# Kernel optimization log

Measured on AMD Instinct MI355X. Metric: run time of the kernel, lower is better.

The kernel has to match this reference:

```python
import jax, jax.numpy as jnp
import numpy as np

B, C, H, G = 4, 128, 8, 64
F = G * G  # 4096 faces on a GxG grid mesh surrogate
DH = C // H


def _build_rings():
    # BFS rings on a GxG 4-neighbor grid from face 0 (corner): ring r = {(i,j): i+j == r}
    rings_list = []
    for r in range(2 * G - 1):
        lo, hi = max(0, r - G + 1), min(r, G - 1)
        rings_list.append([i * G + (r - i) for i in range(lo, hi + 1)])
    n_rings = len(rings_list)
    max_ring = max(len(rr) for rr in rings_list)
    rings = np.full((n_rings, max_ring), -1, dtype=np.int64)
    sizes = np.zeros((n_rings,), dtype=np.int64)
    for r, rr in enumerate(rings_list):
        rings[r, :len(rr)] = rr
        sizes[r] = len(rr)
    return rings, sizes


def setup_inputs() -> dict:
    key = jax.random.key(0)
    ks = jax.random.split(key, 6)
    s = 1.0 / np.sqrt(C)
    x = jax.random.normal(ks[0], (B, C, F), dtype=jnp.float32)
    Wq0 = jax.random.normal(ks[1], (C, C), dtype=jnp.float32) * s
    Wk0 = jax.random.normal(ks[2], (C, C), dtype=jnp.float32) * s
    Wv0 = jax.random.normal(ks[3], (C, C), dtype=jnp.float32) * s
    Wq1 = jax.random.normal(ks[4], (C, C), dtype=jnp.float32) * s
    Wk1 = jax.random.normal(ks[5], (C, C), dtype=jnp.float32) * s
    rings, sizes = _build_rings()
    return {"x": x, "Wq0": Wq0, "Wk0": Wk0, "Wv0": Wv0, "Wq1": Wq1, "Wk1": Wk1,
            "rings": jnp.asarray(rings), "ring_sizes": jnp.asarray(sizes)}


def _attend(q_in, kv_in, Wq, Wk, Wv):
    # AnchorAttentionBlock, mode='resid': MHA(q=q_in, kv=kv_in) + q_in
    Bq, Cc, Nq = q_in.shape
    Nk = kv_in.shape[2]
    q = jnp.einsum('oc,bcn->bon', Wq, q_in).reshape(Bq, H, DH, Nq)
    k = jnp.einsum('oc,bcn->bon', Wk, kv_in).reshape(Bq, H, DH, Nk)
    v = jnp.einsum('oc,bcn->bon', Wv, kv_in).reshape(Bq, H, DH, Nk)
    a = jax.nn.softmax(jnp.einsum('bhdq,bhdk->bhqk', q, k) / np.float32(np.sqrt(DH)), axis=-1)
    o = jnp.einsum('bhqk,bhdk->bhdq', a, v).reshape(Bq, Cc, Nq)
    return o + q_in


def _cos_map(q_in, kv_in, Wq, Wk):
    # return_map=True, normalize=True -> per-head cosine similarity map in [-1, 1]
    Bq, _, Nq = q_in.shape
    Nk = kv_in.shape[2]
    q = jnp.einsum('oc,bcn->bon', Wq, q_in).reshape(Bq, H, DH, Nq)
    k = jnp.einsum('oc,bcn->bon', Wk, kv_in).reshape(Bq, H, DH, Nk)
    qn = q * jax.lax.rsqrt(jnp.sum(q * q, axis=2, keepdims=True) + 1e-8)
    kn = k * jax.lax.rsqrt(jnp.sum(k * k, axis=2, keepdims=True) + 1e-8)
    return jnp.einsum('bhdq,bhdk->bhqk', qn, kn)  # [B,H,Nq,Nk]


def reference(x, Wq0, Wk0, Wv0, Wq1, Wk1, rings, ring_sizes):
    rings_np = np.asarray(rings)
    sizes_np = np.asarray(ring_sizes)
    feats = x
    # Sequential BFS flood-fill: per ring, boundary faces attend over all faces.
    # Vectorized over the batch (all meshes share the grid topology + anchor).
    for r in range(rings_np.shape[0]):
        ring = rings_np[r, :int(sizes_np[r])]          # concrete face indices of this ring
        bf = feats[:, :, ring]                          # [B, C, Nb] boundary features
        bf = _attend(bf, feats, Wq0, Wk0, Wv0)          # kv = all faces (current state)
        feats = feats.at[:, :, ring].set(bf)
    anchor = int(rings_np[0, 0])
    anchor_x = feats[:, :, anchor:anchor + 1]           # [B, C, 1]
    q_x = _attend(x, anchor_x, Wq0, Wk0, Wv0)           # attention[:-1] pass on raw x
    m = _cos_map(q_x, anchor_x, Wq1, Wk1)               # [B, H, F, 1] in [-1, 1]
    final_scores = jnp.mean((m + 1.0) * 0.5, axis=1)    # [B, F, 1] in [0, 1]
    return feats, final_scores
```

## Files before the change

### kernel.cpp

```cpp
#include <hip/hip_runtime.h>
#include <hip/hip_bf16.h>

#define Bn 4
#define Cn 128
#define Fn 4096
#define NRINGS 127

typedef short bhalf4 __attribute__((ext_vector_type(4)));
typedef float f32x4  __attribute__((ext_vector_type(4)));

#define OFF_K   1048576
#define OFF_V   2097152
#define OFF_PM  3145728
#define OFF_PL  3211264
#define OFF_PO  3276800
#define OFF_VA  4325376
#define OFF_KN  4325888

__device__ __forceinline__ ushort f2bf(float f) {
    __hip_bfloat16 h = __float2bfloat16(f);
    return *reinterpret_cast<ushort*>(&h);
}

__global__ __launch_bounds__(512, 2) void initQKV(
    const float* __restrict__ x, const float* __restrict__ Wq0,
    const float* __restrict__ Wk0, const float* __restrict__ Wv0,
    ushort* __restrict__ Q0bf, ushort* __restrict__ Kbf, ushort* __restrict__ Vbf)
{
    __shared__ float xs[Cn * 64];
    const int wg = blockIdx.x, t = threadIdx.x;
    const int b = wg >> 6, n0 = (wg & 63) << 6;
    for (int idx = t; idx < Cn * 64; idx += 512) {
        int c = idx >> 6, j = idx & 63;
        xs[idx] = x[(((b << 7) + c) << 12) + n0 + j];
    }
    __syncthreads();
    const int o = t & 127, j0 = (t >> 7) << 4;
    float aq[16], ak[16], av[16];
#pragma unroll
    for (int k = 0; k < 16; ++k) { aq[k] = 0.f; ak[k] = 0.f; av[k] = 0.f; }
    for (int c = 0; c < Cn; ++c) {
        float wq = Wq0[(o << 7) + c];
        float wk = Wk0[(o << 7) + c];
        float wv = Wv0[(o << 7) + c];
        const float* xr = &xs[(c << 6) + j0];
#pragma unroll
        for (int k = 0; k < 16; ++k) {
            float xv = xr[k];
            aq[k] += wq * xv; ak[k] += wk * xv; av[k] += wv * xv;
        }
    }
    const int h = o >> 4, d = o & 15;
    const int bh = (b << 3) + h;
#pragma unroll
    for (int k = 0; k < 16; ++k) {
        int col = n0 + j0 + k;
        int qi = ((bh << 12) + col) * 16 + d;
        Q0bf[qi] = f2bf(aq[k]);
        Kbf[qi]  = f2bf(ak[k]);
    }
    uint vv[8];
#pragma unroll
    for (int k2 = 0; k2 < 8; ++k2)
        vv[k2] = (uint)f2bf(av[2*k2]) | ((uint)f2bf(av[2*k2+1]) << 16);
    uint4* dst = (uint4*)&Vbf[(((bh << 4) + d) << 12) + n0 + j0];
    dst[0] = make_uint4(vv[0], vv[1], vv[2], vv[3]);
    dst[1] = make_uint4(vv[4], vv[5], vv[6], vv[7]);
}

template<bool TAIL>
__global__ __launch_bounds__(512, 2) void fusedRing(
    const float* __restrict__ x, const float* __restrict__ Wk0,
    const float* __restrict__ Wv0, const int* __restrict__ rings,
    const int* __restrict__ rsz, const ushort* __restrict__ Q0bf,
    ushort* __restrict__ Kbf, ushort* __restrict__ Vbf,
    float* __restrict__ pm, float* __restrict__ pl, float* __restrict__ po,
    float* __restrict__ feats, int r)
{
    __shared__ ushort Kls[512 * 24];
    __shared__ ushort Vls[16 * 520];
    __shared__ ushort Qls[64 * 24];
    __shared__ float  outc[4 * 128];
    __shared__ int colsC[64], colsF[64];
    __shared__ int ownIdx[64];
    __shared__ int ownCnt;

    const int t = threadIdx.x, wgid = blockIdx.x;
    const int b = wgid >> 6, h = (wgid >> 3) & 7, sp = wgid & 7;
    const int bh = (b << 3) + h;
    const int n  = TAIL ? 0 : rsz[r];
    const int np = (r > 0) ? rsz[r - 1] : 0;
    const int keybase = sp << 9;

    if (t < 64) colsC[t] = (r > 0 && t < np) ? rings[(r-1)*64 + t] : -1;
    else if (t < 128) { int q = t - 64; colsF[q] = (!TAIL && q < n) ? rings[r*64 + q] : -1; }
    if (t == 0) ownCnt = 0;
    __syncthreads();

    if (!TAIL) {
        {
            const uint4* src = (const uint4*)(Kbf + ((bh << 12) + keybase + t) * 16);
            uint4 a0 = src[0], a1 = src[1];
            *(uint4*)&Kls[t*24]     = a0;
            *(uint4*)&Kls[t*24 + 8] = a1;
        }
        {
            int d = t >> 5, c32 = t & 31;
            const uint4* src = (const uint4*)(Vbf + (((bh << 4) + d) << 12) + keybase + (c32 << 4));
            uint4 a0 = src[0], a1 = src[1];
            *(uint4*)&Vls[d*520 + (c32 << 4)]     = a0;
            *(uint4*)&Vls[d*520 + (c32 << 4) + 8] = a1;
        }
        if (t < 128) {
            int q = t >> 1, half = t & 1;
            int cq = colsF[q];
            uint4 qv = make_uint4(0u, 0u, 0u, 0u);
            if (cq >= 0)
                qv = *(const uint4*)(Q0bf + ((bh << 12) + cq) * 16 + half * 8);
            *(uint4*)&Qls[q*24 + half*8] = qv;
        }
    }
    __syncthreads();

    if (r > 0) {
        const int bufp = (r - 1) & 1;
        if (t < np) {
            int cq = colsC[t];
            if (cq >= keybase && cq < keybase + 512) {
                int slot = atomicAdd(&ownCnt, 1);
                ownIdx[slot] = t;
            }
        }
        __syncthreads();
        const int cnt = ownCnt;
        for (int base = 0; base < cnt; base += 4) {
            {
                int slot = t >> 7, c = t & 127;
                int ow = base + slot;
                if (ow < cnt) {
                    int j = ownIdx[ow];
                    int col = colsC[j];
                    int hh = c >> 4, dd = c & 15;
                    int p0 = ((bufp << 5) + (b << 3) + hh) * 1024 + j;
                    float mstar = -1e30f;
#pragma unroll
                    for (int s2 = 0; s2 < 16; ++s2)
                        mstar = fmaxf(mstar, pm[p0 + (s2 << 6)]);
                    float lstar = 0.f, osum = 0.f;
#pragma unroll
                    for (int s2 = 0; s2 < 16; ++s2) {
                        int pi = p0 + (s2 << 6);
                        float e = __expf(pm[pi] - mstar);
                        lstar += pl[pi] * e;
                        osum  += po[(pi << 4) + dd] * e;
                    }
                    float outv = osum / lstar + x[(((b << 7) + c) << 12) + col];
                    outc[(slot << 7) + c] = outv;
                    if (h == 0) feats[(((b << 7) + c) << 12) + col] = outv;
                }
            }
            __syncthreads();
            if (!TAIL && t < 128) {
                int slot = t >> 5;
                int ow = base + slot;
                if (ow < cnt) {
                    int task = t & 31;
                    int isV = task >> 4, dd = task & 15;
                    int col = colsC[ownIdx[ow]];
                    const float* W = isV ? Wv0 : Wk0;
                    const float* oc = &outc[slot << 7];
                    int row = (h << 4) + dd;
                    float acc = 0.f;
                    for (int c2 = 0; c2 < Cn; ++c2)
                        acc += W[(row << 7) + c2] * oc[c2];
                    ushort bfv = f2bf(acc);
                    if (isV) {
                        Vbf[(((bh << 4) + dd) << 12) + col] = bfv;
                        Vls[dd*520 + (col - keybase)] = bfv;
                    } else {
                        Kbf[((bh << 12) + col) * 16 + dd] = bfv;
                        Kls[(col - keybase)*24 + dd] = bfv;
                    }
                }
            }
            __syncthreads();
        }
    }
    if (TAIL) return;

    const int w = t >> 6, lane = t & 63;
    const int qt = w & 3, kh = w >> 2;
    const int buf = r & 1;
    if (qt * 16 < n) {
        const int lm = lane & 15, lg = lane >> 4;
        bhalf4 qf = *(const bhalf4*)&Qls[(qt*16 + lm)*24 + (lg << 2)];
        const int key0 = kh << 8;
        f32x4 sc[16];
#pragma unroll
        for (int kt = 0; kt < 16; ++kt) {
            bhalf4 kf = *(const bhalf4*)&Kls[(key0 + (kt << 4) + lm)*24 + (lg << 2)];
            f32x4 z = {0.f, 0.f, 0.f, 0.f};
            sc[kt] = __builtin_amdgcn_mfma_f32_16x16x16bf16_1k(kf, qf, z, 0, 0, 0);
        }
        float m = -1e30f;
#pragma unroll
        for (int kt = 0; kt < 16; ++kt) {
            m = fmaxf(m, fmaxf(fmaxf(sc[kt][0], sc[kt][1]), fmaxf(sc[kt][2], sc[kt][3])));
        }
        m = fmaxf(m, __shfl_xor(m, 16));
        m = fmaxf(m, __shfl_xor(m, 32));
        float lsum = 0.f;
        bhalf4 pf[16];
#pragma unroll
        for (int kt = 0; kt < 16; ++kt) {
            float p0 = __expf((sc[kt][0] - m) * 0.25f);
            float p1 = __expf((sc[kt][1] - m) * 0.25f);
            float p2 = __expf((sc[kt][2] - m) * 0.25f);
            float p3 = __expf((sc[kt][3] - m) * 0.25f);
            lsum += (p0 + p1) + (p2 + p3);
            bhalf4 pv;
            pv[0] = (short)f2bf(p0); pv[1] = (short)f2bf(p1);
            pv[2] = (short)f2bf(p2); pv[3] = (short)f2bf(p3);
            pf[kt] = pv;
        }
        lsum += __shfl_xor(lsum, 16);
        lsum += __shfl_xor(lsum, 32);
        f32x4 oacc = {0.f, 0.f, 0.f, 0.f};
#pragma unroll
        for (int kt = 0; kt < 16; ++kt) {
            bhalf4 vf = *(const bhalf4*)&Vls[lm*520 + key0 + (kt << 4) + (lg << 2)];
            oacc = __builtin_amdgcn_mfma_f32_16x16x16bf16_1k(pf[kt], vf, oacc, 0, 0, 0);
        }
        const int pb = ((((buf << 5) + bh) << 4) | ((sp << 1) + kh)) * 64;
        if (lg == 0) {
            pm[pb + qt*16 + lm] = m * 0.25f;
            pl[pb + qt*16 + lm] = lsum;
        }
#pragma unroll
        for (int reg = 0; reg < 4; ++reg)
            po[(pb + qt*16 + (lg << 2) + reg) * 16 + lm] = oacc[reg];
    }
}

__global__ __launch_bounds__(128) void epi1(
    const float* __restrict__ feats, const float* __restrict__ Wv0,
    const float* __restrict__ Wk1, const int* __restrict__ rings,
    float* __restrict__ Va, float* __restrict__ Kn)
{
    int b = blockIdx.x;
    int i = threadIdx.x;
    int anchor = rings[0];
    __shared__ float la[128];
    __shared__ float kk2[128];
    la[i] = feats[((b * Cn + i) << 12) + anchor];
    __syncthreads();
    float va = 0.f, k1 = 0.f;
    for (int c = 0; c < 128; ++c) {
        va += Wv0[i * 128 + c] * la[c];
        k1 += Wk1[i * 128 + c] * la[c];
    }
    Va[b * 128 + i] = va;
    kk2[i] = k1 * k1;
    __syncthreads();
    float ss = 0.f;
    int hb = i & ~15;
    for (int d = 0; d < 16; ++d) ss += kk2[hb + d];
    Kn[b * 128 + i] = k1 * rsqrtf(ss + 1e-8f);
}

__global__ __launch_bounds__(256) void epi2(
    const float* __restrict__ x, const float* __restrict__ Wq1,
    const float* __restrict__ Va, const float* __restrict__ Kn,
    float* __restrict__ scores)
{
    __shared__ float Wt[128 * 132];
    __shared__ float lxT[128 * 36];
    const int bid = blockIdx.x, t = threadIdx.x;
    const int b = bid >> 7, col0 = (bid & 127) << 5;
    for (int idx = t; idx < 128 * 128; idx += 256) {
        int o = idx >> 7, c = idx & 127;
        Wt[c*132 + o] = Wq1[idx];
    }
    for (int idx = t; idx < 128 * 32; idx += 256) {
        int c = idx >> 5, col = idx & 31;
        lxT[c*36 + col] = x[(((b << 7) + c) << 12) + col0 + col] + Va[(b << 7) + c];
    }
    __syncthreads();
    const int og = t & 31, colg = t >> 5;
    const int o0 = og << 2, cl0 = colg << 2;
    float acc[4][4];
#pragma unroll
    for (int i = 0; i < 4; ++i)
#pragma unroll
        for (int j = 0; j < 4; ++j) acc[i][j] = 0.f;
    for (int c = 0; c < 128; ++c) {
        f32x4 wv = *(const f32x4*)&Wt[c*132 + o0];
        f32x4 xv = *(const f32x4*)&lxT[c*36 + cl0];
#pragma unroll
        for (int i = 0; i < 4; ++i)
#pragma unroll
            for (int j = 0; j < 4; ++j) acc[i][j] += wv[i] * xv[j];
    }
    float kn4[4];
#pragma unroll
    for (int i = 0; i < 4; ++i) kn4[i] = Kn[(b << 7) + o0 + i];
    float res[4];
#pragma unroll
    for (int j = 0; j < 4; ++j) {
        float ss = acc[0][j]*acc[0][j] + acc[1][j]*acc[1][j]
                 + acc[2][j]*acc[2][j] + acc[3][j]*acc[3][j];
        ss += __shfl_xor(ss, 1);
        ss += __shfl_xor(ss, 2);
        float rs = rsqrtf(ss + 1e-8f);
        float mp = (acc[0][j]*kn4[0] + acc[1][j]*kn4[1]
                  + acc[2][j]*kn4[2] + acc[3][j]*kn4[3]) * rs;
#pragma unroll
        for (int msk = 1; msk <= 16; msk <<= 1) mp += __shfl_xor(mp, msk);
        res[j] = 0.5f + mp * (1.0f / 16.0f);
    }
    if (og == 0) {
#pragma unroll
        for (int j = 0; j < 4; ++j)
            scores[(b << 12) + col0 + cl0 + j] = res[j];
    }
}

extern "C" void kernel_launch(void* const* d_in, const int* in_sizes, int n_in,
                              void* d_out, int out_size, void* d_ws, size_t ws_size,
                              hipStream_t stream) {
    const float* x   = (const float*)d_in[0];
    const float* Wq0 = (const float*)d_in[1];
    const float* Wk0 = (const float*)d_in[2];
    const float* Wv0 = (const float*)d_in[3];
    const float* Wq1 = (const float*)d_in[4];
    const float* Wk1 = (const float*)d_in[5];
    const int*   rings = (const int*)d_in[6];
    const int*   rsz   = (const int*)d_in[7];

    float* feats  = (float*)d_out;
    float* scores = feats + Bn * Cn * Fn;

    float*  ws   = (float*)d_ws;
    ushort* Q0bf = (ushort*)ws;
    ushort* Kbf  = (ushort*)(ws + OFF_K);
    ushort* Vbf  = (ushort*)(ws + OFF_V);
    float*  pm   = ws + OFF_PM;
    float*  pl   = ws + OFF_PL;
    float*  po   = ws + OFF_PO;
    float*  Va   = ws + OFF_VA;
    float*  Kn   = ws + OFF_KN;

    initQKV<<<256, 512, 0, stream>>>(x, Wq0, Wk0, Wv0, Q0bf, Kbf, Vbf);

    for (int r = 0; r < NRINGS; ++r) {
        fusedRing<false><<<256, 512, 0, stream>>>(
            x, Wk0, Wv0, rings, rsz, Q0bf, Kbf, Vbf, pm, pl, po, feats, r);
    }
    fusedRing<true><<<256, 512, 0, stream>>>(
        x, Wk0, Wv0, rings, rsz, Q0bf, Kbf, Vbf, pm, pl, po, feats, NRINGS);

    epi1<<<Bn, 128, 0, stream>>>(feats, Wv0, Wk1, rings, Va, Kn);
    epi2<<<512, 256, 0, stream>>>(x, Wq1, Va, Kn, scores);
}
```

Before: 1.781 ms.

## Tile weights in LDS, transpose split-K partials layout, fuse P·V into softmax loop

initQKV now stages the Q/K/V weight slices in shared memory in 32-column chunks and reads x with vector loads, instead of each thread reading weights from global memory. The split-K partial buffers (pm/pl/po) are re-laid out so the 16 splits for one query are contiguous, which lets the merge step use vectorized f32x4 loads. The P·V MFMA is interleaved into the exp loop so the pf[16] register array is no longer needed. Padding query columns now read Q at column 0 instead of a guarded zero, and index math is widened to size_t; this costs extra LDS in initQKV and makes the partial writes strided.

Result: slower. 1.985 ms (+11.5%).

```diff
diff --git a/kernel.cpp b/kernel.cpp
--- a/kernel.cpp
+++ b/kernel.cpp
@@ -28,26 +28,40 @@
     ushort* __restrict__ Q0bf, ushort* __restrict__ Kbf, ushort* __restrict__ Vbf)
 {
     __shared__ float xs[Cn * 64];
+    __shared__ float Wls[3 * 128 * 33];
     const int wg = blockIdx.x, t = threadIdx.x;
     const int b = wg >> 6, n0 = (wg & 63) << 6;
     for (int idx = t; idx < Cn * 64; idx += 512) {
         int c = idx >> 6, j = idx & 63;
-        xs[idx] = x[(((b << 7) + c) << 12) + n0 + j];
-    }
-    __syncthreads();
+        xs[idx] = x[(size_t)((b << 7) + c) * 4096 + n0 + j];
+    }
     const int o = t & 127, j0 = (t >> 7) << 4;
     float aq[16], ak[16], av[16];
 #pragma unroll
     for (int k = 0; k < 16; ++k) { aq[k] = 0.f; ak[k] = 0.f; av[k] = 0.f; }
-    for (int c = 0; c < Cn; ++c) {
-        float wq = Wq0[(o << 7) + c];
-        float wk = Wk0[(o << 7) + c];
-        float wv = Wv0[(o << 7) + c];
-        const float* xr = &xs[(c << 6) + j0];
-#pragma unroll
-        for (int k = 0; k < 16; ++k) {
-            float xv = xr[k];
-            aq[k] += wq * xv; ak[k] += wk * xv; av[k] += wv * xv;
+    for (int cc = 0; cc < 128; cc += 32) {
+        __syncthreads();
+        for (int idx = t; idx < 128 * 32; idx += 512) {
+            int oo = idx >> 5, jj = idx & 31;
+            Wls[oo * 33 + jj]                = Wq0[(oo << 7) + cc + jj];
+            Wls[128 * 33 + oo * 33 + jj]     = Wk0[(oo << 7) + cc + jj];
+            Wls[2 * 128 * 33 + oo * 33 + jj] = Wv0[(oo << 7) + cc + jj];
+        }
+        __syncthreads();
+        for (int c2 = 0; c2 < 32; ++c2) {
+            float wq = Wls[o * 33 + c2];
+            float wk = Wls[128 * 33 + o * 33 + c2];
+            float wv = Wls[2 * 128 * 33 + o * 33 + c2];
+            const f32x4* xr4 = (const f32x4*)&xs[((cc + c2) << 6) + j0];
+#pragma unroll
+            for (int k4 = 0; k4 < 4; ++k4) {
+                f32x4 xv = xr4[k4];
+#pragma unroll
+                for (int e = 0; e < 4; ++e) {
+                    int k = (k4 << 2) + e;
+                    aq[k] += wq * xv[e]; ak[k] += wk * xv[e]; av[k] += wv * xv[e];
+                }
+            }
         }
     }
     const int h = o >> 4, d = o & 15;
@@ -55,7 +69,7 @@
 #pragma unroll
     for (int k = 0; k < 16; ++k) {
         int col = n0 + j0 + k;
-        int qi = ((bh << 12) + col) * 16 + d;
+        size_t qi = (size_t)(bh * 4096 + col) * 16 + d;
         Q0bf[qi] = f2bf(aq[k]);
         Kbf[qi]  = f2bf(ak[k]);
     }
@@ -63,7 +77,7 @@
 #pragma unroll
     for (int k2 = 0; k2 < 8; ++k2)
         vv[k2] = (uint)f2bf(av[2*k2]) | ((uint)f2bf(av[2*k2+1]) << 16);
-    uint4* dst = (uint4*)&Vbf[(((bh << 4) + d) << 12) + n0 + j0];
+    uint4* dst = (uint4*)&Vbf[(size_t)(bh * 16 + d) * 4096 + n0 + j0];
     dst[0] = make_uint4(vv[0], vv[1], vv[2], vv[3]);
     dst[1] = make_uint4(vv[4], vv[5], vv[6], vv[7]);
 }
@@ -93,20 +107,20 @@
     const int keybase = sp << 9;
 
     if (t < 64) colsC[t] = (r > 0 && t < np) ? rings[(r-1)*64 + t] : -1;
-    else if (t < 128) { int q = t - 64; colsF[q] = (!TAIL && q < n) ? rings[r*64 + q] : -1; }
+    else if (t < 128) { int q = t - 64; colsF[q] = (!TAIL && q < n) ? rings[r*64 + q] : 0; }
     if (t == 0) ownCnt = 0;
     __syncthreads();
 
     if (!TAIL) {
         {
-            const uint4* src = (const uint4*)(Kbf + ((bh << 12) + keybase + t) * 16);
+            const uint4* src = (const uint4*)(Kbf + (size_t)((bh << 12) + keybase + t) * 16);
             uint4 a0 = src[0], a1 = src[1];
             *(uint4*)&Kls[t*24]     = a0;
             *(uint4*)&Kls[t*24 + 8] = a1;
         }
         {
             int d = t >> 5, c32 = t & 31;
-            const uint4* src = (const uint4*)(Vbf + (((bh << 4) + d) << 12) + keybase + (c32 << 4));
+            const uint4* src = (const uint4*)(Vbf + (size_t)(bh*16 + d) * 4096 + keybase + (c32 << 4));
             uint4 a0 = src[0], a1 = src[1];
             *(uint4*)&Vls[d*520 + (c32 << 4)]     = a0;
             *(uint4*)&Vls[d*520 + (c32 << 4) + 8] = a1;
@@ -114,9 +128,7 @@
         if (t < 128) {
             int q = t >> 1, half = t & 1;
             int cq = colsF[q];
-            uint4 qv = make_uint4(0u, 0u, 0u, 0u);
-            if (cq >= 0)
-                qv = *(const uint4*)(Q0bf + ((bh << 12) + cq) * 16 + half * 8);
+            uint4 qv = *(const uint4*)(Q0bf + (size_t)((bh << 12) + cq) * 16 + half * 8);
             *(uint4*)&Qls[q*24 + half*8] = qv;
         }
     }
@@ -141,22 +153,41 @@
                     int j = ownIdx[ow];
                     int col = colsC[j];
                     int hh = c >> 4, dd = c & 15;
-                    int p0 = ((bufp << 5) + (b << 3) + hh) * 1024 + j;
-                    float mstar = -1e30f;
-#pragma unroll
-                    for (int s2 = 0; s2 < 16; ++s2)
-                        mstar = fmaxf(mstar, pm[p0 + (s2 << 6)]);
-                    float lstar = 0.f, osum = 0.f;
-#pragma unroll
-                    for (int s2 = 0; s2 < 16; ++s2) {
-                        int pi = p0 + (s2 << 6);
-                        float e = __expf(pm[pi] - mstar);
-                        lstar += pl[pi] * e;
-                        osum  += po[(pi << 4) + dd] * e;
+                    int bhh = (b << 3) + hh;
+                    int qb = ((((bufp << 5) + bhh) << 6) + j) << 4;
+                    f32x4 m0 = *(const f32x4*)&pm[qb];
+                    f32x4 m1 = *(const f32x4*)&pm[qb + 4];
+                    f32x4 m2 = *(const f32x4*)&pm[qb + 8];
+                    f32x4 m3 = *(const f32x4*)&pm[qb + 12];
+                    float mstar = fmaxf(
+                        fmaxf(fmaxf(fmaxf(m0[0],m0[1]),fmaxf(m0[2],m0[3])),
+                              fmaxf(fmaxf(m1[0],m1[1]),fmaxf(m1[2],m1[3]))),
+                        fmaxf(fmaxf(fmaxf(m2[0],m2[1]),fmaxf(m2[2],m2[3])),
+                              fmaxf(fmaxf(m3[0],m3[1]),fmaxf(m3[2],m3[3]))));
+                    f32x4 l0 = *(const f32x4*)&pl[qb];
+                    f32x4 l1 = *(const f32x4*)&pl[qb + 4];
+                    f32x4 l2 = *(const f32x4*)&pl[qb + 8];
+                    f32x4 l3 = *(const f32x4*)&pl[qb + 12];
+                    int pob = (qb + dd) << 4;
+                    f32x4 o0 = *(const f32x4*)&po[pob];
+                    f32x4 o1 = *(const f32x4*)&po[pob + 4];
+                    f32x4 o2 = *(const f32x4*)&po[pob + 8];
+                    f32x4 o3 = *(const f32x4*)&po[pob + 12];
+                    float lst = 0.f, osum = 0.f;
+#pragma unroll
+                    for (int s2 = 0; s2 < 4; ++s2) {
+                        float e0 = __expf(m0[s2] - mstar);
+                        lst += l0[s2] * e0; osum += o0[s2] * e0;
+                        float e1 = __expf(m1[s2] - mstar);
+                        lst += l1[s2] * e1; osum += o1[s2] * e1;
+                        float e2 = __expf(m2[s2] - mstar);
+                        lst += l2[s2] * e2; osum += o2[s2] * e2;
+                        float e3 = __expf(m3[s2] - mstar);
+                        lst += l3[s2] * e3; osum += o3[s2] * e3;
                     }
-                    float outv = osum / lstar + x[(((b << 7) + c) << 12) + col];
+                    float outv = osum / lst + x[(size_t)((b << 7) + c) * 4096 + col];
                     outc[(slot << 7) + c] = outv;
-                    if (h == 0) feats[(((b << 7) + c) << 12) + col] = outv;
+                    if (h == 0) feats[(size_t)((b << 7) + c) * 4096 + col] = outv;
                 }
             }
             __syncthreads();
@@ -175,10 +206,10 @@
                         acc += W[(row << 7) + c2] * oc[c2];
                     ushort bfv = f2bf(acc);
                     if (isV) {
-                        Vbf[(((bh << 4) + dd) << 12) + col] = bfv;
+                        Vbf[(size_t)(bh*16 + dd) * 4096 + col] = bfv;
                         Vls[dd*520 + (col - keybase)] = bfv;
                     } else {
-                        Kbf[((bh << 12) + col) * 16 + dd] = bfv;
+                        Kbf[(size_t)((bh << 12) + col) * 16 + dd] = bfv;
                         Kls[(col - keybase)*24 + dd] = bfv;
                     }
                 }
@@ -204,13 +235,12 @@
         }
         float m = -1e30f;
 #pragma unroll
-        for (int kt = 0; kt < 16; ++kt) {
+        for (int kt = 0; kt < 16; ++kt)
             m = fmaxf(m, fmaxf(fmaxf(sc[kt][0], sc[kt][1]), fmaxf(sc[kt][2], sc[kt][3])));
-        }
         m = fmaxf(m, __shfl_xor(m, 16));
         m = fmaxf(m, __shfl_xor(m, 32));
         float lsum = 0.f;
-        bhalf4 pf[16];
+        f32x4 oacc = {0.f, 0.f, 0.f, 0.f};
 #pragma unroll
         for (int kt = 0; kt < 16; ++kt) {
             float p0 = __expf((sc[kt][0] - m) * 0.25f);
@@ -221,24 +251,22 @@
             bhalf4 pv;
             pv[0] = (short)f2bf(p0); pv[1] = (short)f2bf(p1);
             pv[2] = (short)f2bf(p2); pv[3] = (short)f2bf(p3);
-            pf[kt] = pv;
+            bhalf4 vf = *(const bhalf4*)&Vls[lm*520 + key0 + (kt << 4) + (lg << 2)];
+            oacc = __builtin_amdgcn_mfma_f32_16x16x16bf16_1k(pv, vf, oacc, 0, 0, 0);
         }
         lsum += __shfl_xor(lsum, 16);
         lsum += __shfl_xor(lsum, 32);
-        f32x4 oacc = {0.f, 0.f, 0.f, 0.f};
-#pragma unroll
-        for (int kt = 0; kt < 16; ++kt) {
-            bhalf4 vf = *(const bhalf4*)&Vls[lm*520 + key0 + (kt << 4) + (lg << 2)];
-            oacc = __builtin_amdgcn_mfma_f32_16x16x16bf16_1k(pf[kt], vf, oacc, 0, 0, 0);
-        }
-        const int pb = ((((buf << 5) + bh) << 4) | ((sp << 1) + kh)) * 64;
+        const int sl = (sp << 1) + kh;
+        const int qbase = (((buf << 5) + bh) << 6) + qt * 16;
         if (lg == 0) {
-            pm[pb + qt*16 + lm] = m * 0.25f;
-            pl[pb + qt*16 + lm] = lsum;
-        }
-#pragma unroll
-        for (int reg = 0; reg < 4; ++reg)
-            po[(pb + qt*16 + (lg << 2) + reg) * 16 + lm] = oacc[reg];
+            pm[((qbase + lm) << 4) + sl] = m * 0.25f;
+            pl[((qbase + lm) << 4) + sl] = lsum;
+        }
+#pragma unroll
+        for (int reg = 0; reg < 4; ++reg) {
+            int q = qbase + (lg << 2) + reg;
+            po[(((q << 4) + lm) << 4) + sl] = oacc[reg];
+        }
     }
 }
 
@@ -252,7 +280,7 @@
     int anchor = rings[0];
     __shared__ float la[128];
     __shared__ float kk2[128];
-    la[i] = feats[((b * Cn + i) << 12) + anchor];
+    la[i] = feats[(size_t)((b << 7) + i) * 4096 + anchor];
     __syncthreads();
     float va = 0.f, k1 = 0.f;
     for (int c = 0; c < 128; ++c) {
@@ -283,7 +311,7 @@
     }
     for (int idx = t; idx < 128 * 32; idx += 256) {
         int c = idx >> 5, col = idx & 31;
-        lxT[c*36 + col] = x[(((b << 7) + c) << 12) + col0 + col] + Va[(b << 7) + c];
+        lxT[c*36 + col] = x[(size_t)((b << 7) + c) * 4096 + col0 + col] + Va[(b << 7) + c];
     }
     __syncthreads();
     const int og = t & 31, colg = t >> 5;
```
